# Optimization experiments

Measured on AMD Instinct MI355X. Metric: run time of the kernel, lower is better.

Reference implementation:

```python
import jax, jax.numpy as jnp
from jax import lax
import numpy as np

PAD = 3
COEFF_POS = jnp.array([-2.0, 15.0, -60.0, 20.0, 30.0, -3.0]) / 60.0
COEFF_NEG = jnp.array([3.0, -30.0, -20.0, 60.0, -15.0, 2.0]) / 60.0
EPI_TOL = 1e-5
N_TERMS = 19  # k = 1..19 as in the torch loop


def geo_cyclic_pad(x, p=PAD):
    # Cyclic in longitude; across the poles: flip latitude and shift lon by 180 deg.
    W = x.shape[-1]
    top = jnp.flip(jnp.roll(x[:, :, :p, :], W // 2, axis=-1), axis=2)
    bot = jnp.flip(jnp.roll(x[:, :, -p:, :], W // 2, axis=-1), axis=2)
    x = jnp.concatenate([top, x, bot], axis=2)
    return jnp.concatenate([x[..., -p:], x, x[..., :p]], axis=-1)


def _corr6(x, k, axis):
    # cross-correlation with a length-6 kernel along `axis` (== F.conv2d with 1x6/6x1 kernel)
    n = x.shape[axis] - 5
    out = k[0] * lax.slice_in_dim(x, 0, n, axis=axis)
    for j in range(1, 6):
        out = out + k[j] * lax.slice_in_dim(x, j, j + n, axis=axis)
    return out


def upwind_derivative(q_padded, velocity, dx, axis):
    # 5th-order upwind finite difference with sign-dependent stencil selection
    H, W = velocity.shape[2], velocity.shape[3]
    cp = COEFF_POS.astype(q_padded.dtype)
    cn = COEFF_NEG.astype(q_padded.dtype)
    d_pos = _corr6(q_padded, cp, axis)
    d_neg = _corr6(q_padded, cn, axis)
    if axis == 3:  # longitude
        d_pos = d_pos[:, :, PAD:-PAD, :W]
        d_neg = d_neg[:, :, PAD:-PAD, 1:W + 1]
    else:  # latitude (axis == 2)
        d_pos = d_pos[:, :, :H, PAD:-PAD]
        d_neg = d_neg[:, :, 1:H + 1, PAD:-PAD]
    return jnp.where(velocity > 0, d_pos, d_neg) / dx


def compute_rhs(q, u, v, dlat, dlon):
    qp = geo_cyclic_pad(q)
    dq_dlon = upwind_derivative(qp, u, dlon, axis=3)
    dq_dlat = upwind_derivative(qp, v, dlat, axis=2)
    return -u * dq_dlon - v * dq_dlat


def phi1_times_vector(dt, rhs_fn, vector):
    # phi_1(dt*J) v = v + sum_{k>=1} (dt J)^k / (k+1)! v ; early break when term max-norm < tol
    def step(carry, k):
        term, result, done = carry
        new_term = rhs_fn(term) * (dt / (k + 1.0))
        small = jnp.max(jnp.abs(new_term)) < EPI_TOL
        term = jnp.where(done, term, new_term)
        result = jnp.where(done | small, result, result + new_term)
        return (term, result, done | small), None
    ks = jnp.arange(1, N_TERMS + 1, dtype=vector.dtype)
    (_, result, _), _ = lax.scan(step, (vector, vector, jnp.array(False)), ks)
    return result


def setup_inputs() -> dict:
    key = jax.random.key(0)
    ks = jax.random.split(key, 9)
    B, hidden_dim, num_vels = 1, 256, 16
    H, W = 181, 360  # ERA5 1-degree grid
    hidden_features = jax.random.normal(ks[0], (B, hidden_dim, H, W), jnp.float32)
    u = jax.random.normal(ks[1], (B, num_vels, H, W), jnp.float32)
    v = jax.random.normal(ks[2], (B, num_vels, H, W), jnp.float32)
    lat = jnp.linspace(-jnp.pi / 2, jnp.pi / 2, H)
    lon = jnp.linspace(0.0, 2.0 * jnp.pi, W, endpoint=False)
    dlat = (lat[1] - lat[0]).astype(jnp.float32)
    dlon = (lon[1] - lon[0]).astype(jnp.float32)
    dt = jnp.float32(1e-3)  # small enough that the Taylor series converges below EPI_TOL
    W_down = jax.random.normal(ks[3], (num_vels, hidden_dim), jnp.float32) * (1.0 / np.sqrt(hidden_dim))
    b_down = jax.random.normal(ks[4], (num_vels,), jnp.float32) * 0.01
    dw = jax.random.normal(ks[5], (num_vels,), jnp.float32)
    db = jax.random.normal(ks[6], (num_vels,), jnp.float32) * 0.01
    W_up = jax.random.normal(ks[7], (hidden_dim, num_vels), jnp.float32) * (1.0 / np.sqrt(num_vels))
    b_up = jax.random.normal(ks[8], (hidden_dim,), jnp.float32) * 0.01
    return {"hidden_features": hidden_features, "u": u, "v": v, "dt": dt,
            "dlat": dlat, "dlon": dlon, "W_down": W_down, "b_down": b_down,
            "dw": dw, "db": db, "W_up": W_up, "b_up": b_up}


def reference(hidden_features, u, v, dt, dlat, dlon, W_down, b_down, dw, db, W_up, b_up):
    # down projection (CLinear == 1x1 conv)
    q = jnp.einsum('oc,bchw->bohw', W_down, hidden_features) + b_down[None, :, None, None]
    F_n = compute_rhs(q, u, v, dlat, dlon)
    rhs_fn = lambda vec: compute_rhs(vec, u, v, dlat, dlon)  # Jacobian action (rhs is linear in q)
    phi1_F = phi1_times_vector(dt, rhs_fn, F_n)
    updated = q + phi1_F * dt
    # up projection (SepConv k=1 == depthwise 1x1 then pointwise 1x1)
    dwc = updated * dw[None, :, None, None] + db[None, :, None, None]
    return jnp.einsum('oc,bchw->bohw', W_up, dwc) + b_up[None, :, None, None]
```

## Files before the change

### kernel.cpp

```cpp
#include <hip/hip_runtime.h>
#include <hip/hip_fp16.h>

#define HH 181
#define WW 360
#define NPIX (HH*WW)
#define NCH 16
#define NHID 256
#define NPIX16 (NCH*NPIX)
#define NG4 (NPIX16/4)
#define NPG4 (NPIX/4)
#define GPR (WW/4)
#define GPC (NPIX/4)
#define NPASS 6

typedef __attribute__((ext_vector_type(8))) short bf16x8;
typedef __attribute__((ext_vector_type(4))) float f32x4;

__device__ __forceinline__ unsigned short f2bf(float x) {
    union { float f; unsigned u; } c; c.f = x;
    unsigned r = c.u + 0x7FFFu + ((c.u >> 16) & 1u);
    return (unsigned short)(r >> 16);
}

__device__ __forceinline__ void h4tof(const void* p, float* f) {
    uint2 t = *(const uint2*)p;
    union { unsigned w; __half2 h; } a, b;
    a.w = t.x; b.w = t.y;
    float2 f01 = __half22float2(a.h), f23 = __half22float2(b.h);
    f[0] = f01.x; f[1] = f01.y; f[2] = f23.x; f[3] = f23.y;
}

__global__ __launch_bounds__(256) void prep_kernel(
        const float* __restrict__ Wd, unsigned short* __restrict__ WdB,
        const float* __restrict__ u, const float* __restrict__ v,
        const float* __restrict__ dlon_p, const float* __restrict__ dlat_p,
        unsigned* __restrict__ uvh) {
    if (blockIdx.x == 0) {
        for (int t = threadIdx.x; t < NCH * NHID; t += 256)
            WdB[t] = f2bf(Wd[t]);
    }
    const int i4 = blockIdx.x * 256 + threadIdx.x;
    if (i4 >= NG4) return;
    const float il = 1.0f / dlon_p[0], ia = 1.0f / dlat_p[0];
    float4 U = ((const float4*)u)[i4];
    float4 V = ((const float4*)v)[i4];
    union { __half2 h; unsigned w; } c0, c1, c2, c3;
    c0.h = __floats2half2_rn(U.x * il, V.x * ia);
    c1.h = __floats2half2_rn(U.y * il, V.y * ia);
    c2.h = __floats2half2_rn(U.z * il, V.z * ia);
    c3.h = __floats2half2_rn(U.w * il, V.w * ia);
    ((uint4*)uvh)[i4] = make_uint4(c0.w, c1.w, c2.w, c3.w);
}

__global__ __launch_bounds__(256) void down_kernel(const float* __restrict__ hid,
                                                   const unsigned short* __restrict__ WdB,
                                                   const float* __restrict__ b_down,
                                                   float* __restrict__ q) {
    const int lid = threadIdx.x & 63, wid = threadIdx.x >> 6;
    const int col = lid & 15;
    const int g   = lid >> 4;
    const int pix0 = blockIdx.x * 64 + wid * 16;
    const int pix  = min(pix0 + col, NPIX - 1);

    bf16x8 a[8];
#pragma unroll
    for (int kk = 0; kk < 8; ++kk)
        a[kk] = *(const bf16x8*)(WdB + col * NHID + kk * 32 + g * 8);

    f32x4 acc;
#pragma unroll
    for (int r = 0; r < 4; ++r) acc[r] = b_down[g * 4 + r];

    float braw[8][8];
#pragma unroll
    for (int kk = 0; kk < 8; ++kk)
#pragma unroll
        for (int j = 0; j < 8; ++j)
            braw[kk][j] = hid[(size_t)(kk * 32 + g * 8 + j) * NPIX + pix];

#pragma unroll
    for (int kk = 0; kk < 8; ++kk) {
        bf16x8 b;
#pragma unroll
        for (int j = 0; j < 8; ++j) b[j] = (short)f2bf(braw[kk][j]);
        acc = __builtin_amdgcn_mfma_f32_16x16x32_bf16(a[kk], b, acc, 0, 0, 0);
    }

    if (pix0 + col < NPIX) {
#pragma unroll
        for (int r = 0; r < 4; ++r)
            q[(g * 4 + r) * NPIX + pix0 + col] = acc[r];
    }
}

__global__ __launch_bounds__(256) void pass_kernel(
        const float* __restrict__ qin,
        const unsigned* __restrict__ tin,
        unsigned* __restrict__ tout,
        const unsigned* __restrict__ uvh,
        float* __restrict__ result,
        const float* __restrict__ dt_p,
        int k) {
    const float cp0 = -2.0f/60.0f, cp1 = 15.0f/60.0f, cp2 = -60.0f/60.0f,
                cp3 = 20.0f/60.0f, cp4 = 30.0f/60.0f, cp5 = -3.0f/60.0f;
    const float cn0 =  3.0f/60.0f, cn1 = -30.0f/60.0f, cn2 = -20.0f/60.0f,
                cn3 = 60.0f/60.0f, cn4 = -15.0f/60.0f, cn5 =  2.0f/60.0f;

    const int g4 = blockIdx.x * 256 + threadIdx.x;
    if (g4 >= NG4) return;
    const float scale = (k == 0) ? 1.0f : dt_p[0] / (float)(k + 1);

    const int ch  = g4 / GPC;
    const int rem = g4 - ch * GPC;
    const int h   = rem / GPR;
    const int bi  = rem - h * GPR;
    const int w0  = bi * 4;
    const int wf0 = (w0 >= WW / 2) ? (w0 - WW / 2) : (w0 + WW / 2);

    float Wn[12];
    float S[7][4];
    if (k == 0) {
        const float* base = qin + ch * NPIX;
        const float4* rowv = (const float4*)(base + h * WW);
        float4 Af = rowv[bi == 0 ? GPR - 1 : bi - 1];
        float4 Bf = rowv[bi];
        float4 Cf = rowv[bi == GPR - 1 ? 0 : bi + 1];
        Wn[0]=Af.x; Wn[1]=Af.y; Wn[2]=Af.z; Wn[3]=Af.w;
        Wn[4]=Bf.x; Wn[5]=Bf.y; Wn[6]=Bf.z; Wn[7]=Bf.w;
        Wn[8]=Cf.x; Wn[9]=Cf.y; Wn[10]=Cf.z; Wn[11]=Cf.w;
#pragma unroll
        for (int d = 0; d < 7; ++d) {
            int rr = h + d - 3, cb = w0;
            if (rr < 0)           { rr = -1 - rr;        cb = wf0; }
            else if (rr > HH - 1) { rr = 2*HH - 1 - rr;  cb = wf0; }
            float4 t = *(const float4*)(base + rr * WW + cb);
            S[d][0]=t.x; S[d][1]=t.y; S[d][2]=t.z; S[d][3]=t.w;
        }
    } else {
        const __half* base = (const __half*)tin + (size_t)ch * NPIX;
        const __half* row = base + h * WW;
        h4tof(row + (bi == 0 ? GPR - 1 : bi - 1) * 4, Wn);
        h4tof(row + bi * 4, Wn + 4);
        h4tof(row + (bi == GPR - 1 ? 0 : bi + 1) * 4, Wn + 8);
#pragma unroll
        for (int d = 0; d < 7; ++d) {
            int rr = h + d - 3, cb = w0;
            if (rr < 0)           { rr = -1 - rr;        cb = wf0; }
            else if (rr > HH - 1) { rr = 2*HH - 1 - rr;  cb = wf0; }
            h4tof(base + rr * WW + cb, S[d]);
        }
    }

    const int gi = ch * NPIX + h * WW + w0;
    const uint4 P = *(const uint4*)(uvh + gi);
    const unsigned Pw[4] = {P.x, P.y, P.z, P.w};

    float o4[4];
#pragma unroll
    for (int j = 0; j < 4; ++j) {
        float dpl = cp0*Wn[j+1] + cp1*Wn[j+2] + cp2*Wn[j+3]
                  + cp3*Wn[j+4] + cp4*Wn[j+5] + cp5*Wn[j+6];
        float dnl = cn0*Wn[j+2] + cn1*Wn[j+3] + cn2*Wn[j+4]
                  + cn3*Wn[j+5] + cn4*Wn[j+6] + cn5*Wn[j+7];
        float dpa = cp0*S[0][j] + cp1*S[1][j] + cp2*S[2][j]
                  + cp3*S[3][j] + cp4*S[4][j] + cp5*S[5][j];
        float dna = cn0*S[1][j] + cn1*S[2][j] + cn2*S[3][j]
                  + cn3*S[4][j] + cn4*S[5][j] + cn5*S[6][j];
        union { unsigned w; __half2 h; } cv; cv.w = Pw[j];
        float uu = __low2float(cv.h);
        float vv = __high2float(cv.h);
        o4[j] = (-uu * (uu > 0.0f ? dpl : dnl)
                 -vv * (vv > 0.0f ? dpa : dna)) * scale;
    }

    if (k < NPASS - 1) {
        __half2 p01 = __floats2half2_rn(o4[0], o4[1]);
        __half2 p23 = __floats2half2_rn(o4[2], o4[3]);
        union { __half2 h; unsigned w; } q01, q23; q01.h = p01; q23.h = p23;
        *(uint2*)((__half*)tout + gi) = make_uint2(q01.w, q23.w);
    }

    if (k == 0) {
        *(float4*)(result + gi) = make_float4(o4[0], o4[1], o4[2], o4[3]);
    } else if (k == NPASS - 1) {
        float4 R = *(const float4*)(result + gi);
        R.x += o4[0]; R.y += o4[1]; R.z += o4[2]; R.w += o4[3];
        *(float4*)(result + gi) = R;
    } else if ((k & 1) == 0) {
        float4 R = *(const float4*)(result + gi);
        R.x += Wn[4] + o4[0]; R.y += Wn[5] + o4[1];
        R.z += Wn[6] + o4[2]; R.w += Wn[7] + o4[3];
        *(float4*)(result + gi) = R;
    }
}

__global__ __launch_bounds__(256) void up_kernel(const float* __restrict__ q,
                                                 const float* __restrict__ result,
                                                 const float* __restrict__ dt_p,
                                                 const float* __restrict__ dw,
                                                 const float* __restrict__ db,
                                                 const float* __restrict__ Wu,
                                                 const float* __restrict__ b_up,
                                                 float* __restrict__ out) {
    const int g = blockIdx.x * 256 + threadIdx.x;
    if (g >= NPG4) return;
    const int pix0 = g * 4;
    const int c0 = blockIdx.y * 32;
    const float dt = dt_p[0];

    float d[NCH][4];
#pragma unroll
    for (int o = 0; o < NCH; ++o) {
        const int gb = o * NPIX + pix0;
        float4 Q = *(const float4*)(q + gb);
        float4 R = *(const float4*)(result + gb);
        float dwo = dw[o], dbo = db[o];
        d[o][0] = (Q.x + R.x * dt) * dwo + dbo;
        d[o][1] = (Q.y + R.y * dt) * dwo + dbo;
        d[o][2] = (Q.z + R.z * dt) * dwo + dbo;
        d[o][3] = (Q.w + R.w * dt) * dwo + dbo;
    }
#pragma unroll 4
    for (int cc = 0; cc < 32; ++cc) {
        const int c = c0 + cc;
        const float bc = b_up[c];
        float a0 = bc, a1 = bc, a2 = bc, a3 = bc;
#pragma unroll
        for (int o = 0; o < NCH; ++o) {
            float wv = Wu[c * NCH + o];
            a0 += wv * d[o][0]; a1 += wv * d[o][1];
            a2 += wv * d[o][2]; a3 += wv * d[o][3];
        }
        *(float4*)(out + c * NPIX + pix0) = make_float4(a0, a1, a2, a3);
    }
}

extern "C" void kernel_launch(void* const* d_in, const int* in_sizes, int n_in,
                              void* d_out, int out_size, void* d_ws, size_t ws_size,
                              hipStream_t stream) {
    const float* hidden = (const float*)d_in[0];
    const float* u      = (const float*)d_in[1];
    const float* v      = (const float*)d_in[2];
    const float* dt_p   = (const float*)d_in[3];
    const float* dlat_p = (const float*)d_in[4];
    const float* dlon_p = (const float*)d_in[5];
    const float* W_down = (const float*)d_in[6];
    const float* b_down = (const float*)d_in[7];
    const float* dw     = (const float*)d_in[8];
    const float* db     = (const float*)d_in[9];
    const float* W_up   = (const float*)d_in[10];
    const float* b_up   = (const float*)d_in[11];
    float* out = (float*)d_out;

    float* ws = (float*)d_ws;
    float* q      = ws;
    float* result = ws + (size_t)NPIX16;
    unsigned* t0  = (unsigned*)(ws + (size_t)2 * NPIX16);
    unsigned* t1  = t0 + (size_t)NPIX16 / 2;
    unsigned short* WdB = (unsigned short*)(ws + (size_t)3 * NPIX16);
    unsigned* uvh = (unsigned*)out;

    const int nbg = (NG4 + 255) / 256;
    const int nbu = (NPG4 + 255) / 256;
    const int nbd = (NPIX + 63) / 64;

    prep_kernel<<<nbg, 256, 0, stream>>>(W_down, WdB, u, v, dlon_p, dlat_p, uvh);
    down_kernel<<<nbd, 256, 0, stream>>>(hidden, WdB, b_down, q);

    pass_kernel<<<nbg, 256, 0, stream>>>(q, t1, t0, uvh, result, dt_p, 0);
    for (int k = 1; k < NPASS; ++k) {
        unsigned* tin  = (k & 1) ? t0 : t1;
        unsigned* tout = (k & 1) ? t1 : t0;
        pass_kernel<<<nbg, 256, 0, stream>>>(q, tin, tout, uvh, result, dt_p, k);
    }

    up_kernel<<<dim3(nbu, 8), 256, 0, stream>>>(q, result, dt_p, dw, db,
                                                W_up, b_up, out);
}
```

Baseline: 85.16 us.

## Fuse prep into down-projection kernel and store phi1 accumulator in fp16

Removes the separate prep kernel. Each down-projection block now converts the fp32 W_down tile to bf16 itself and also packs its slice of the u/v velocity pairs to half precision. Block size drops to 128 threads covering 32 pixels, which doubles the block count. The phi1 result accumulator changes from fp32 to fp16, halving its read/write traffic in every pass and in the up-projection, but accumulating in half precision risks accuracy loss.

```diff
diff --git a/kernel.cpp b/kernel.cpp
--- a/kernel.cpp
+++ b/kernel.cpp
@@ -30,42 +30,42 @@
     f[0] = f01.x; f[1] = f01.y; f[2] = f23.x; f[3] = f23.y;
 }
 
-__global__ __launch_bounds__(256) void prep_kernel(
-        const float* __restrict__ Wd, unsigned short* __restrict__ WdB,
-        const float* __restrict__ u, const float* __restrict__ v,
-        const float* __restrict__ dlon_p, const float* __restrict__ dlat_p,
+__device__ __forceinline__ void f4toh(void* p, float a, float b, float c, float d) {
+    union { __half2 h; unsigned w; } x, y;
+    x.h = __floats2half2_rn(a, b);
+    y.h = __floats2half2_rn(c, d);
+    *(uint2*)p = make_uint2(x.w, y.w);
+}
+
+__global__ __launch_bounds__(128) void down_kernel(
+        const float* __restrict__ hid,
+        const float* __restrict__ Wd,
+        const float* __restrict__ b_down,
+        const float* __restrict__ u,
+        const float* __restrict__ v,
+        const float* __restrict__ dlon_p,
+        const float* __restrict__ dlat_p,
+        float* __restrict__ q,
         unsigned* __restrict__ uvh) {
-    if (blockIdx.x == 0) {
-        for (int t = threadIdx.x; t < NCH * NHID; t += 256)
-            WdB[t] = f2bf(Wd[t]);
-    }
-    const int i4 = blockIdx.x * 256 + threadIdx.x;
-    if (i4 >= NG4) return;
-    const float il = 1.0f / dlon_p[0], ia = 1.0f / dlat_p[0];
-    float4 U = ((const float4*)u)[i4];
-    float4 V = ((const float4*)v)[i4];
-    union { __half2 h; unsigned w; } c0, c1, c2, c3;
-    c0.h = __floats2half2_rn(U.x * il, V.x * ia);
-    c1.h = __floats2half2_rn(U.y * il, V.y * ia);
-    c2.h = __floats2half2_rn(U.z * il, V.z * ia);
-    c3.h = __floats2half2_rn(U.w * il, V.w * ia);
-    ((uint4*)uvh)[i4] = make_uint4(c0.w, c1.w, c2.w, c3.w);
-}
-
-__global__ __launch_bounds__(256) void down_kernel(const float* __restrict__ hid,
-                                                   const unsigned short* __restrict__ WdB,
-                                                   const float* __restrict__ b_down,
-                                                   float* __restrict__ q) {
     const int lid = threadIdx.x & 63, wid = threadIdx.x >> 6;
     const int col = lid & 15;
     const int g   = lid >> 4;
-    const int pix0 = blockIdx.x * 64 + wid * 16;
+    const int pix0 = blockIdx.x * 32 + wid * 16;
     const int pix  = min(pix0 + col, NPIX - 1);
 
     bf16x8 a[8];
 #pragma unroll
-    for (int kk = 0; kk < 8; ++kk)
-        a[kk] = *(const bf16x8*)(WdB + col * NHID + kk * 32 + g * 8);
+    for (int kk = 0; kk < 8; ++kk) {
+        const float* wp = Wd + col * NHID + kk * 32 + g * 8;
+        float4 w0 = *(const float4*)wp;
+        float4 w1 = *(const float4*)(wp + 4);
+        bf16x8 t;
+        t[0] = (short)f2bf(w0.x); t[1] = (short)f2bf(w0.y);
+        t[2] = (short)f2bf(w0.z); t[3] = (short)f2bf(w0.w);
+        t[4] = (short)f2bf(w1.x); t[5] = (short)f2bf(w1.y);
+        t[6] = (short)f2bf(w1.z); t[7] = (short)f2bf(w1.w);
+        a[kk] = t;
+    }
 
     f32x4 acc;
 #pragma unroll
@@ -90,6 +90,21 @@
 #pragma unroll
         for (int r = 0; r < 4; ++r)
             q[(g * 4 + r) * NPIX + pix0 + col] = acc[r];
+    }
+
+    const float il = 1.0f / dlon_p[0], ia = 1.0f / dlat_p[0];
+    const int px0b = blockIdx.x * 32;
+#pragma unroll
+    for (int it = 0; it < 4; ++it) {
+        int idx = it * 128 + threadIdx.x;
+        int ch  = idx >> 5;
+        int px  = px0b + (idx & 31);
+        if (px < NPIX) {
+            int gidx = ch * NPIX + px;
+            union { __half2 h; unsigned w; } cv;
+            cv.h = __floats2half2_rn(u[gidx] * il, v[gidx] * ia);
+            uvh[gidx] = cv.w;
+        }
     }
 }
 
@@ -98,7 +113,7 @@
         const unsigned* __restrict__ tin,
         unsigned* __restrict__ tout,
         const unsigned* __restrict__ uvh,
-        float* __restrict__ result,
+        unsigned* __restrict__ result,
         const float* __restrict__ dt_p,
         int k) {
     const float cp0 = -2.0f/60.0f, cp1 = 15.0f/60.0f, cp2 = -60.0f/60.0f,
@@ -173,29 +188,24 @@
                  -vv * (vv > 0.0f ? dpa : dna)) * scale;
     }
 
-    if (k < NPASS - 1) {
-        __half2 p01 = __floats2half2_rn(o4[0], o4[1]);
-        __half2 p23 = __floats2half2_rn(o4[2], o4[3]);
-        union { __half2 h; unsigned w; } q01, q23; q01.h = p01; q23.h = p23;
-        *(uint2*)((__half*)tout + gi) = make_uint2(q01.w, q23.w);
-    }
-
+    if (k < NPASS - 1)
+        f4toh((__half*)tout + gi, o4[0], o4[1], o4[2], o4[3]);
+
+    __half* rp = (__half*)result + gi;
     if (k == 0) {
-        *(float4*)(result + gi) = make_float4(o4[0], o4[1], o4[2], o4[3]);
+        f4toh(rp, o4[0], o4[1], o4[2], o4[3]);
     } else if (k == NPASS - 1) {
-        float4 R = *(const float4*)(result + gi);
-        R.x += o4[0]; R.y += o4[1]; R.z += o4[2]; R.w += o4[3];
-        *(float4*)(result + gi) = R;
+        float r4[4]; h4tof(rp, r4);
+        f4toh(rp, r4[0]+o4[0], r4[1]+o4[1], r4[2]+o4[2], r4[3]+o4[3]);
     } else if ((k & 1) == 0) {
-        float4 R = *(const float4*)(result + gi);
-        R.x += Wn[4] + o4[0]; R.y += Wn[5] + o4[1];
-        R.z += Wn[6] + o4[2]; R.w += Wn[7] + o4[3];
-        *(float4*)(result + gi) = R;
+        float r4[4]; h4tof(rp, r4);
+        f4toh(rp, r4[0]+Wn[4]+o4[0], r4[1]+Wn[5]+o4[1],
+                  r4[2]+Wn[6]+o4[2], r4[3]+Wn[7]+o4[3]);
     }
 }
 
 __global__ __launch_bounds__(256) void up_kernel(const float* __restrict__ q,
-                                                 const float* __restrict__ result,
+                                                 const unsigned* __restrict__ result,
                                                  const float* __restrict__ dt_p,
                                                  const float* __restrict__ dw,
                                                  const float* __restrict__ db,
@@ -213,12 +223,12 @@
     for (int o = 0; o < NCH; ++o) {
         const int gb = o * NPIX + pix0;
         float4 Q = *(const float4*)(q + gb);
-        float4 R = *(const float4*)(result + gb);
+        float r4[4]; h4tof((const __half*)result + gb, r4);
         float dwo = dw[o], dbo = db[o];
-        d[o][0] = (Q.x + R.x * dt) * dwo + dbo;
-        d[o][1] = (Q.y + R.y * dt) * dwo + dbo;
-        d[o][2] = (Q.z + R.z * dt) * dwo + dbo;
-        d[o][3] = (Q.w + R.w * dt) * dwo + dbo;
+        d[o][0] = (Q.x + r4[0] * dt) * dwo + dbo;
+        d[o][1] = (Q.y + r4[1] * dt) * dwo + dbo;
+        d[o][2] = (Q.z + r4[2] * dt) * dwo + dbo;
+        d[o][3] = (Q.w + r4[3] * dt) * dwo + dbo;
     }
 #pragma unroll 4
     for (int cc = 0; cc < 32; ++cc) {
@@ -253,19 +263,18 @@
     float* out = (float*)d_out;
 
     float* ws = (float*)d_ws;
-    float* q      = ws;
-    float* result = ws + (size_t)NPIX16;
-    unsigned* t0  = (unsigned*)(ws + (size_t)2 * NPIX16);
-    unsigned* t1  = t0 + (size_t)NPIX16 / 2;
-    unsigned short* WdB = (unsigned short*)(ws + (size_t)3 * NPIX16);
-    unsigned* uvh = (unsigned*)out;
+    float* q          = ws;
+    unsigned* result  = (unsigned*)(ws + (size_t)NPIX16);
+    unsigned* t0      = (unsigned*)(ws + (size_t)NPIX16 + NPIX16/2);
+    unsigned* t1      = (unsigned*)(ws + (size_t)2 * NPIX16);
+    unsigned* uvh     = (unsigned*)out;
 
     const int nbg = (NG4 + 255) / 256;
     const int nbu = (NPG4 + 255) / 256;
-    const int nbd = (NPIX + 63) / 64;
-
-    prep_kernel<<<nbg, 256, 0, stream>>>(W_down, WdB, u, v, dlon_p, dlat_p, uvh);
-    down_kernel<<<nbd, 256, 0, stream>>>(hidden, WdB, b_down, q);
+    const int nbd = (NPIX + 31) / 32;
+
+    down_kernel<<<nbd, 128, 0, stream>>>(hidden, W_down, b_down, u, v,
+                                         dlon_p, dlat_p, q, uvh);
 
     pass_kernel<<<nbg, 256, 0, stream>>>(q, t1, t0, uvh, result, dt_p, 0);
     for (int k = 1; k < NPASS; ++k) {
```

New measurement: 84.64 us. Within noise of the previous version (-0.6%).
